# Optimization experiments

Measured on AMD Instinct MI355X. Metric: run time of the kernel, lower is better.

## Reference

```python
import jax, jax.numpy as jnp
import numpy as np

B, C, CO, H, W = 64, 64, 64, 56, 56
E, K = 8, 2


def _conv3x3(x, k, b):
    # x: [B,C,H,W], k: [CO,C,3,3], b: [CO]
    y = jax.lax.conv_general_dilated(
        x, k, window_strides=(1, 1), padding='SAME',
        dimension_numbers=('NCHW', 'OIHW', 'NCHW'))
    return y + b[None, :, None, None]


def setup_inputs() -> dict:
    key = jax.random.key(0)
    k1, k2, k3, k4, k5 = jax.random.split(key, 5)
    x = jax.random.normal(k1, (B, C, H, W), dtype=jnp.float32)
    weights = jax.random.uniform(k2, (B, K), dtype=jnp.float32)
    indices = jax.random.randint(k3, (B, K), 0, E, dtype=jnp.int32)
    W_exp = jax.random.normal(k4, (E, CO, C, 3, 3), dtype=jnp.float32) * 0.05
    b_exp = jax.random.normal(k5, (E, CO), dtype=jnp.float32) * 0.01
    return {'x': x, 'weights': weights, 'indices': indices,
            'W_exp': W_exp, 'b_exp': b_exp}


def reference(x, weights, indices, W_exp, b_exp):
    # Dense-equivalent MoE dispatch: run every expert on the full batch,
    # then gather the top-k expert outputs per sample and combine.
    # Same math as the masked gather / index_add_ loop in the torch module.
    # acts: [E, B, CO, H, W]
    acts = jax.vmap(lambda k, b: jax.nn.relu(_conv3x3(x, k, b)))(W_exp, b_exp)
    acts_b = jnp.transpose(acts, (1, 0, 2, 3, 4))  # [B, E, CO, H, W]
    idx = indices[:, :, None, None, None].astype(jnp.int32)
    sel = jnp.take_along_axis(acts_b, idx, axis=1)  # [B, K, CO, H, W]
    out = jnp.sum(sel * weights[:, :, None, None, None], axis=1)  # [B, CO, H, W]
    return out
```

## Files before the change

### kernel.cpp

```cpp
#include <hip/hip_runtime.h>


#define BB 64
#define CC 64
#define COO 64
#define HH 56
#define WW 56

typedef __bf16 bf16x8 __attribute__((ext_vector_type(8)));
typedef float  f32x4  __attribute__((ext_vector_type(4)));

__global__ __launch_bounds__(256) void prep_kernel(
    const float* __restrict__ x, const float* __restrict__ Wexp,
    __bf16* __restrict__ xT, __bf16* __restrict__ Wpack)
{
    const int bx  = blockIdx.x;
    const int tid = threadIdx.x;

    if (bx < 3712) {
        const int b  = bx / 58;
        const int hp = bx - b * 58;
        __bf16* dst = xT + ((size_t)b * 58 + hp) * 4224;

        if (hp == 0 || hp == 57) {
            bf16x8 z = {};
            for (int j = tid; j < 528; j += 256)
                *(bf16x8*)(dst + j * 8) = z;
            return;
        }

        __shared__ __align__(16) float tile[CC * WW];
        const int h = hp - 1;
        const float* xb = x + ((size_t)b * CC * HH + h) * WW;

        for (int i = tid; i < 896; i += 256) {
            const int c = i / 14, wq = i - c * 14;
            const f32x4 f = *(const f32x4*)(xb + (size_t)c * (HH * WW) + wq * 4);
            *(f32x4*)&tile[i * 4] = f;
        }
        __syncthreads();

        for (int j = tid; j < 528; j += 256) {
            const int cg = j / 66, wc = j - cg * 66;
            bf16x8 v = {};
            if (wc >= 1 && wc <= WW) {
                #pragma unroll
                for (int u = 0; u < 8; ++u)
                    v[u] = (__bf16)tile[(cg * 8 + u) * WW + (wc - 1)];
            }
            *(bf16x8*)(dst + j * 8) = v;
        }
    } else {
        const int wp = bx - 3712;
        const int e  = wp / 9, rs = wp - e * 9;
        const int r  = rs / 3, s  = rs - r * 3;
        for (int idx = tid; idx < 4096; idx += 256) {
            const int ks   = idx >> 11;
            const int rem  = idx & 2047;
            const int mt   = rem >> 9;
            const int lane = (rem >> 3) & 63;
            const int j    = idx & 7;
            const int co = mt * 16 + (lane & 15);
            const int c  = ks * 32 + ((lane >> 4) << 3) + j;
            const float v = Wexp[((((size_t)e * COO + co) * CC + c) * 3 + r) * 3 + s];
            Wpack[(size_t)e * 36864 + (size_t)rs * 4096 + idx] = (__bf16)v;
        }
    }
}

__global__ __launch_bounds__(256, 3) void moe_conv_mfma(
    const __bf16* __restrict__ xT, const __bf16* __restrict__ Wpack,
    const float* __restrict__ gate_w, const int* __restrict__ gate_i,
    const float* __restrict__ bexp, float* __restrict__ out)
{
    __shared__ __align__(16) __bf16 ldsA[2 * 6144];

    const int bid = blockIdx.x;
    const int swz = (bid & 7) * 224 + (bid >> 3);
    const int b   = swz / 28;
    const int rem = swz - b * 28;
    const int h0  = (rem >> 1) * 4;
    const int mh  = rem & 1;

    const int tid = threadIdx.x;
    const int wid = tid >> 6, lane = tid & 63;
    const int n15 = lane & 15, quad = lane >> 4;
    const int wcol = wid * 16 + n15;

    const int   e0 = gate_i[b * 2 + 0], e1 = gate_i[b * 2 + 1];
    const float g0 = gate_w[b * 2 + 0], g1 = gate_w[b * 2 + 1];
    const __bf16* w0 = Wpack + (size_t)e0 * 36864;
    const __bf16* w1 = Wpack + (size_t)e1 * 36864;

    auto stage = [&](int g, int bufn) {
        const int s = g >> 1, ks = g & 1;
        #pragma unroll
        for (int i = 0; i < 3; ++i) {
            const int ch = wid * 3 + i;
            const int r = ch >> 2, rm = ch & 3;
            const int slot = rm >> 1, mtl = rm & 1;
            const __bf16* src = (slot ? w1 : w0) + (size_t)(r * 3 + s) * 4096
                              + ks * 2048 + (mh * 2 + mtl) * 512 + lane * 8;
            __bf16* dstp = &ldsA[bufn * 6144 + ch * 512 + lane * 8];
            __builtin_amdgcn_global_load_lds(
                (const __attribute__((address_space(1))) unsigned int*)src,
                (__attribute__((address_space(3))) unsigned int*)dstp, 16, 0, 0);
        }
    };

    const __bf16* pqh = xT + (size_t)b * 244992 + (size_t)h0 * 4224
                      + quad * 528 + wcol * 8;

    f32x4 acc[2][2][4] = {};
    f32x4 bfb[2][6];

    auto issueB = [&](int g, int bufn) {
        const int s = g >> 1, ks = g & 1;
        #pragma unroll
        for (int t = 0; t < 6; ++t) {
            const __bf16* a = pqh + (size_t)t * 4224 + s * 8 + ks * 2112;
            asm volatile("global_load_dwordx4 %0, %1, off"
                         : "=&v"(bfb[bufn][t]) : "v"(a));
        }
    };

    stage(0, 0);
    issueB(0, 0);

    #pragma unroll
    for (int g = 0; g < 6; ++g) {
        const int buf = g & 1;
        asm volatile("s_waitcnt vmcnt(0)" ::: "memory");
        __builtin_amdgcn_sched_barrier(0);
        __builtin_amdgcn_s_barrier();
        __builtin_amdgcn_sched_barrier(0);
        if (g < 5) { stage(g + 1, buf ^ 1); issueB(g + 1, buf ^ 1); }
        __builtin_amdgcn_sched_barrier(0);

        __builtin_amdgcn_s_setprio(1);
        #pragma unroll
        for (int r = 0; r < 3; ++r) {
            #pragma unroll
            for (int slot = 0; slot < 2; ++slot) {
                #pragma unroll
                for (int mtl = 0; mtl < 2; ++mtl) {
                    const bf16x8 af = *(const bf16x8*)
                        &ldsA[buf * 6144 + (r * 4 + slot * 2 + mtl) * 512
                              + lane * 8];
                    #pragma unroll
                    for (int t = 0; t < 4; ++t)
                        acc[slot][mtl][t] = __builtin_amdgcn_mfma_f32_16x16x32_bf16(
                            af, __builtin_bit_cast(bf16x8, bfb[buf][r + t]),
                            acc[slot][mtl][t], 0, 0, 0);
                }
            }
        }
        __builtin_amdgcn_s_setprio(0);
    }

    if (wcol < WW) {
        #pragma unroll
        for (int t = 0; t < 4; ++t) {
            const int h = h0 + t;
            #pragma unroll
            for (int mtl = 0; mtl < 2; ++mtl) {
                #pragma unroll
                for (int v = 0; v < 4; ++v) {
                    const int co = (mh * 2 + mtl) * 16 + quad * 4 + v;
                    float a0 = acc[0][mtl][t][v] + bexp[e0 * COO + co];
                    float a1 = acc[1][mtl][t][v] + bexp[e1 * COO + co];
                    a0 = fmaxf(a0, 0.f);
                    a1 = fmaxf(a1, 0.f);
                    out[(((size_t)b * COO + co) * HH + h) * WW + wcol] =
                        g0 * a0 + g1 * a1;
                }
            }
        }
    }
}

extern "C" void kernel_launch(void* const* d_in, const int* in_sizes, int n_in,
                              void* d_out, int out_size, void* d_ws, size_t ws_size,
                              hipStream_t stream) {
    const float* x      = (const float*)d_in[0];
    const float* gate_w = (const float*)d_in[1];
    const int*   gate_i = (const int*)  d_in[2];
    const float* Wexp   = (const float*)d_in[3];
    const float* bexp   = (const float*)d_in[4];
    float* out = (float*)d_out;

    __bf16* Wpack = (__bf16*)d_ws;
    __bf16* xT    = (__bf16*)((char*)d_ws + 589824);

    prep_kernel<<<dim3(3784), 256, 0, stream>>>(x, Wexp, xT, Wpack);
    moe_conv_mfma<<<dim3(1792), 256, 0, stream>>>(xT, Wpack, gate_w, gate_i,
                                                  bexp, out);
}
```

Baseline: 140.5 us.

## Preload all expert weights to LDS once and triple-buffer input fragments

Stages all 72 weight chunks for the block into LDS with a single upfront async load instead of double-buffered per-step staging, removing the per-iteration block barriers. Input B fragments are now held in a 3-deep register ring with two steps of prefetch and graded vmcnt waits. This raises LDS use to 72 KB and register pressure, so launch bounds drop from 3 to 2 blocks per CU, which reduces occupancy.

```diff
diff --git a/kernel.cpp b/kernel.cpp
--- a/kernel.cpp
+++ b/kernel.cpp
@@ -68,12 +68,12 @@
     }
 }
 
-__global__ __launch_bounds__(256, 3) void moe_conv_mfma(
+__global__ __launch_bounds__(256, 2) void moe_conv_mfma(
     const __bf16* __restrict__ xT, const __bf16* __restrict__ Wpack,
     const float* __restrict__ gate_w, const int* __restrict__ gate_i,
     const float* __restrict__ bexp, float* __restrict__ out)
 {
-    __shared__ __align__(16) __bf16 ldsA[2 * 6144];
+    __shared__ __align__(16) __bf16 ldsA[72 * 512];
 
     const int bid = blockIdx.x;
     const int swz = (bid & 7) * 224 + (bid >> 3);
@@ -92,49 +92,54 @@
     const __bf16* w0 = Wpack + (size_t)e0 * 36864;
     const __bf16* w1 = Wpack + (size_t)e1 * 36864;
 
-    auto stage = [&](int g, int bufn) {
-        const int s = g >> 1, ks = g & 1;
-        #pragma unroll
-        for (int i = 0; i < 3; ++i) {
-            const int ch = wid * 3 + i;
-            const int r = ch >> 2, rm = ch & 3;
-            const int slot = rm >> 1, mtl = rm & 1;
-            const __bf16* src = (slot ? w1 : w0) + (size_t)(r * 3 + s) * 4096
-                              + ks * 2048 + (mh * 2 + mtl) * 512 + lane * 8;
-            __bf16* dstp = &ldsA[bufn * 6144 + ch * 512 + lane * 8];
-            __builtin_amdgcn_global_load_lds(
-                (const __attribute__((address_space(1))) unsigned int*)src,
-                (__attribute__((address_space(3))) unsigned int*)dstp, 16, 0, 0);
-        }
-    };
+    #pragma unroll
+    for (int i = 0; i < 18; ++i) {
+        const int q    = wid * 18 + i;
+        const int rs   = q >> 3;
+        const int rm   = q & 7;
+        const int slot = rm >> 2, ks = (rm >> 1) & 1, mtl = rm & 1;
+        const __bf16* src = (slot ? w1 : w0) + (size_t)rs * 4096
+                          + ks * 2048 + (mh * 2 + mtl) * 512 + lane * 8;
+        __bf16* dstp = &ldsA[q * 512 + lane * 8];
+        __builtin_amdgcn_global_load_lds(
+            (const __attribute__((address_space(1))) unsigned int*)src,
+            (__attribute__((address_space(3))) unsigned int*)dstp, 16, 0, 0);
+    }
 
     const __bf16* pqh = xT + (size_t)b * 244992 + (size_t)h0 * 4224
                       + quad * 528 + wcol * 8;
 
     f32x4 acc[2][2][4] = {};
-    f32x4 bfb[2][6];
-
-    auto issueB = [&](int g, int bufn) {
-        const int s = g >> 1, ks = g & 1;
+    f32x4 bfb[3][6];
+
+    auto issueB = [&](int m) {
+        const int s = m >> 1, ks = m & 1, mb = m % 3;
         #pragma unroll
         for (int t = 0; t < 6; ++t) {
             const __bf16* a = pqh + (size_t)t * 4224 + s * 8 + ks * 2112;
             asm volatile("global_load_dwordx4 %0, %1, off"
-                         : "=&v"(bfb[bufn][t]) : "v"(a));
+                         : "=&v"(bfb[mb][t]) : "v"(a));
         }
     };
 
-    stage(0, 0);
-    issueB(0, 0);
+    issueB(0);
+    issueB(1);
+    asm volatile("s_waitcnt vmcnt(12)" ::: "memory");
+    __builtin_amdgcn_sched_barrier(0);
+    __builtin_amdgcn_s_barrier();
+    __builtin_amdgcn_sched_barrier(0);
 
     #pragma unroll
     for (int g = 0; g < 6; ++g) {
-        const int buf = g & 1;
-        asm volatile("s_waitcnt vmcnt(0)" ::: "memory");
-        __builtin_amdgcn_sched_barrier(0);
-        __builtin_amdgcn_s_barrier();
-        __builtin_amdgcn_sched_barrier(0);
-        if (g < 5) { stage(g + 1, buf ^ 1); issueB(g + 1, buf ^ 1); }
+        const int s = g >> 1, ks = g & 1, buf = g % 3;
+        if (g <= 3) {
+            issueB(g + 2);
+            asm volatile("s_waitcnt vmcnt(12)" ::: "memory");
+        } else if (g == 4) {
+            asm volatile("s_waitcnt vmcnt(6)" ::: "memory");
+        } else {
+            asm volatile("s_waitcnt vmcnt(0)" ::: "memory");
+        }
         __builtin_amdgcn_sched_barrier(0);
 
         __builtin_amdgcn_s_setprio(1);
@@ -145,7 +150,7 @@
                 #pragma unroll
                 for (int mtl = 0; mtl < 2; ++mtl) {
                     const bf16x8 af = *(const bf16x8*)
-                        &ldsA[buf * 6144 + (r * 4 + slot * 2 + mtl) * 512
+                        &ldsA[(((r * 3 + s) * 8) + slot * 4 + ks * 2 + mtl) * 512
                               + lane * 8];
                     #pragma unroll
                     for (int t = 0; t < 4; ++t)
```

After: 142.4 us. Within noise of the previous version (+1.3%).
